# Optimization experiments

Measured on AMD Instinct MI355X. Metric: run time of the kernel, lower is better.

The kernel has to match this reference:

```python
import jax, jax.numpy as jnp
import numpy as np

B, H, KLEN, D = 32, 8, 8192, 64  # batch, heads, kv_len, head_dim


def setup_inputs() -> dict:
    key = jax.random.key(0)
    k1, k2, k3, k4 = jax.random.split(key, 4)
    std = 1.0 / D ** 0.5
    Q = jax.random.normal(k1, (B, H, 1, D), dtype=jnp.float32)
    K = jax.random.normal(k2, (B, H, KLEN, D), dtype=jnp.float32)
    W_c = jax.random.normal(k3, (H, 2 * D, D), dtype=jnp.float32) * std
    W_o = jax.random.normal(k4, (H, D, 1), dtype=jnp.float32) * std
    bias = jnp.zeros((H, 1, D), dtype=jnp.float32)
    return {"Q": Q, "K": K, "W_c": W_c, "W_o": W_o, "bias": bias}


def reference(Q, K, W_c, W_o, bias):
    # concat score (NAIS, He et al. 2018)
    Qe = jnp.broadcast_to(Q, K.shape)                       # [b,h,k,d]
    QK_cat = jnp.concatenate([Qe, K], axis=-1)              # [b,h,k,2d]
    hidden = jax.nn.relu(
        jnp.einsum('bhke,hed->bhkd', QK_cat, W_c) + bias    # bias [h,1,d] broadcasts
    )                                                        # [b,h,k,d]
    scores = jnp.einsum('bhkd,hde->bhk', hidden, W_o)       # sums over d and e(=1)
    return scores
```

## Files before the change

kernel.cpp:

```cpp
#include <hip/hip_runtime.h>
#include <stdint.h>

#define B_    32
#define H_    8
#define KLEN_ 8192
#define D_    64
#define SPLIT 16
#define ROWS_PER_BLOCK (KLEN_ / SPLIT)
#define WAVES 4
#define TILES (ROWS_PER_BLOCK / (WAVES * 16))

#define LDS_ROW 144

typedef __attribute__((ext_vector_type(8))) short short8;
typedef __attribute__((ext_vector_type(4))) float float4v;
typedef __attribute__((ext_vector_type(4))) unsigned int uint4v;
typedef __attribute__((ext_vector_type(2))) unsigned int uint2v;

static __device__ inline unsigned int pack_bf16(float x0, float x1) {
    unsigned int a = __builtin_bit_cast(unsigned int, x0) + 0x8000u;
    unsigned int b = __builtin_bit_cast(unsigned int, x1) + 0x8000u;
    return __builtin_amdgcn_perm(b, a, 0x07060302u);
}

__global__ __launch_bounds__(256) void nais_score_kernel(
    const float* __restrict__ Q,
    const float* __restrict__ K,
    const float* __restrict__ Wc,
    const float* __restrict__ Wo,
    const float* __restrict__ bias,
    float* __restrict__ out)
{
    const int blk   = blockIdx.x;
    const int bh    = blk / SPLIT;
    const int split = blk % SPLIT;
    const int h     = bh % H_;
    const int tid   = threadIdx.x;
    const int lane  = tid & 63;
    const int wave  = tid >> 6;
    const int c     = lane & 15;
    const int q     = lane >> 4;

    __shared__ float s_qb[D_];
    __shared__ float s_wo[D_];
    __shared__ unsigned char s_tile[WAVES][16 * LDS_ROW] __attribute__((aligned(16)));

    if (tid < D_) {
        const float* qv = Q + (size_t)bh * D_;
        const float* wq = Wc + (size_t)h * (2 * D_ * D_);
        float acc = bias[h * D_ + tid];
        #pragma unroll 8
        for (int e = 0; e < D_; ++e)
            acc += qv[e] * wq[e * D_ + tid];
        s_qb[tid] = acc;
        s_wo[tid] = Wo[h * D_ + tid];
    }
    __syncthreads();

    const float* wk = Wc + (size_t)h * (2 * D_ * D_) + D_ * D_;
    short8 bfrag[4][2];
    #pragma unroll
    for (int t = 0; t < 4; ++t) {
        const int d = t * 16 + c;
        #pragma unroll
        for (int half = 0; half < 2; ++half) {
            uint4v f;
            #pragma unroll
            for (int j2 = 0; j2 < 4; ++j2) {
                const int e = half * 32 + q * 8 + 2 * j2;
                f[j2] = pack_bf16(wk[(size_t)e * D_ + d], wk[(size_t)(e + 1) * D_ + d]);
            }
            bfrag[t][half] = __builtin_bit_cast(short8, f);
        }
    }

    float qbl[4], wol[4];
    #pragma unroll
    for (int t = 0; t < 4; ++t) {
        qbl[t] = s_qb[t * 16 + c];
        wol[t] = s_wo[t * 16 + c];
    }

    const float* Kb = K + (size_t)bh * KLEN_ * D_ + (size_t)split * ROWS_PER_BLOCK * D_;
    float*       ob = out + (size_t)bh * KLEN_ + (size_t)split * ROWS_PER_BLOCK;
    unsigned char* myTile = s_tile[wave];

    #define TILE_PTR(t) (Kb + (size_t)(((t) * WAVES + wave) * 16) * D_)

    float4v st[2][4];
    #pragma unroll
    for (int j = 0; j < 4; ++j)
        st[0][j] = *(const float4v*)(TILE_PTR(0) + j * 256 + lane * 4);

    for (int t = 0; t < TILES; ++t) {
        const int cb = t & 1, nb = cb ^ 1;
        if (t + 1 < TILES) {
            #pragma unroll
            for (int j = 0; j < 4; ++j)
                st[nb][j] = *(const float4v*)(TILE_PTR(t + 1) + j * 256 + lane * 4);
        }

        #pragma unroll
        for (int j = 0; j < 4; ++j) {
            const int r = j * 4 + q;
            uint2v w;
            w[0] = pack_bf16(st[cb][j][0], st[cb][j][1]);
            w[1] = pack_bf16(st[cb][j][2], st[cb][j][3]);
            *(uint2v*)(myTile + r * LDS_ROW + c * 8) = w;
        }

        short8 af0 = *(const short8*)(myTile + c * LDS_ROW + q * 16);
        short8 af1 = *(const short8*)(myTile + c * LDS_ROW + 64 + q * 16);

        float4v pr = {0.f, 0.f, 0.f, 0.f};
        #pragma unroll
        for (int tt = 0; tt < 4; ++tt) {
            float4v acc = {0.f, 0.f, 0.f, 0.f};
            acc = __builtin_amdgcn_mfma_f32_16x16x32_bf16(af0, bfrag[tt][0], acc, 0, 0, 0);
            acc = __builtin_amdgcn_mfma_f32_16x16x32_bf16(af1, bfrag[tt][1], acc, 0, 0, 0);
            #pragma unroll
            for (int r = 0; r < 4; ++r) {
                float hv = fmaxf(acc[r] + qbl[tt], 0.f);
                pr[r] += hv * wol[tt];
            }
        }

        const int krow = (t * WAVES + wave) * 16;
        #pragma unroll
        for (int r = 0; r < 4; ++r) {
            float v = pr[r];
            v += __shfl_xor(v, 1);
            v += __shfl_xor(v, 2);
            v += __shfl_xor(v, 4);
            v += __shfl_xor(v, 8);
            if (c == r) ob[krow + q * 4 + r] = v;
        }
    }
    #undef TILE_PTR
}

extern "C" void kernel_launch(void* const* d_in, const int* in_sizes, int n_in,
                              void* d_out, int out_size, void* d_ws, size_t ws_size,
                              hipStream_t stream) {
    const float* Q    = (const float*)d_in[0];
    const float* K    = (const float*)d_in[1];
    const float* Wc   = (const float*)d_in[2];
    const float* Wo   = (const float*)d_in[3];
    const float* bias = (const float*)d_in[4];
    float* out = (float*)d_out;

    dim3 grid(B_ * H_ * SPLIT);
    dim3 block(256);
    nais_score_kernel<<<grid, block, 0, stream>>>(Q, K, Wc, Wo, bias, out);
}
```

Measured before the change: 689.1 us.

## Load K fragments directly into MFMA layout, drop LDS staging and syncthreads

```diff
diff --git a/kernel.cpp b/kernel.cpp
--- a/kernel.cpp
+++ b/kernel.cpp
@@ -9,13 +9,12 @@
 #define ROWS_PER_BLOCK (KLEN_ / SPLIT)
 #define WAVES 4
 #define TILES (ROWS_PER_BLOCK / (WAVES * 16))
+#define TSTRIDE (WAVES * 16 * D_)
 
-#define LDS_ROW 144
-
-typedef __attribute__((ext_vector_type(8))) short short8;
-typedef __attribute__((ext_vector_type(4))) float float4v;
+typedef __attribute__((ext_vector_type(8))) short  short8;
+typedef __attribute__((ext_vector_type(8))) float  float8;
+typedef __attribute__((ext_vector_type(4))) float  float4v;
 typedef __attribute__((ext_vector_type(4))) unsigned int uint4v;
-typedef __attribute__((ext_vector_type(2))) unsigned int uint2v;
 
 static __device__ inline unsigned int pack_bf16(float x0, float x1) {
     unsigned int a = __builtin_bit_cast(unsigned int, x0) + 0x8000u;
@@ -23,7 +22,14 @@
     return __builtin_amdgcn_perm(b, a, 0x07060302u);
 }
 
-__global__ __launch_bounds__(256) void nais_score_kernel(
+static __device__ inline short8 pack8(float8 f) {
+    uint4v p;
+    #pragma unroll
+    for (int j = 0; j < 4; ++j) p[j] = pack_bf16(f[2 * j], f[2 * j + 1]);
+    return __builtin_bit_cast(short8, p);
+}
+
+__global__ __launch_bounds__(256, 4) void nais_score_kernel(
     const float* __restrict__ Q,
     const float* __restrict__ K,
     const float* __restrict__ Wc,
@@ -41,23 +47,38 @@
     const int c     = lane & 15;
     const int q     = lane >> 4;
 
-    __shared__ float s_qb[D_];
-    __shared__ float s_wo[D_];
-    __shared__ unsigned char s_tile[WAVES][16 * LDS_ROW] __attribute__((aligned(16)));
+    const float* Kb    = K + (size_t)bh * (KLEN_ * D_) + (size_t)split * (ROWS_PER_BLOCK * D_);
+    const float* lanep = Kb + (size_t)(wave * 16 + c) * D_ + q * 8;
 
-    if (tid < D_) {
-        const float* qv = Q + (size_t)bh * D_;
-        const float* wq = Wc + (size_t)h * (2 * D_ * D_);
-        float acc = bias[h * D_ + tid];
-        #pragma unroll 8
-        for (int e = 0; e < D_; ++e)
-            acc += qv[e] * wq[e * D_ + tid];
-        s_qb[tid] = acc;
-        s_wo[tid] = Wo[h * D_ + tid];
+    float8 f0[2], f1[2];
+    #pragma unroll
+    for (int p = 0; p < 2; ++p) {
+        f0[p] = *(const float8*)(lanep + p * TSTRIDE);
+        f1[p] = *(const float8*)(lanep + p * TSTRIDE + 32);
     }
-    __syncthreads();
 
-    const float* wk = Wc + (size_t)h * (2 * D_ * D_) + D_ * D_;
+    const float* qv = Q  + (size_t)bh * D_;
+    const float* wq = Wc + (size_t)h * (2 * D_ * D_);
+    const float* wk = wq + D_ * D_;
+
+    float a0 = bias[h * D_ + lane], a1 = 0.f, a2 = 0.f, a3 = 0.f;
+    #pragma unroll
+    for (int e = 0; e < D_; e += 4) {
+        a0 += qv[e]     * wq[(e)     * D_ + lane];
+        a1 += qv[e + 1] * wq[(e + 1) * D_ + lane];
+        a2 += qv[e + 2] * wq[(e + 2) * D_ + lane];
+        a3 += qv[e + 3] * wq[(e + 3) * D_ + lane];
+    }
+    const float qp       = (a0 + a1) + (a2 + a3);
+    const float wol_lane = Wo[h * D_ + lane];
+
+    float qbl[4], wol[4];
+    #pragma unroll
+    for (int tt = 0; tt < 4; ++tt) {
+        qbl[tt] = __shfl(qp,       tt * 16 + c);
+        wol[tt] = __shfl(wol_lane, tt * 16 + c);
+    }
+
     short8 bfrag[4][2];
     #pragma unroll
     for (int t = 0; t < 4; ++t) {
@@ -74,69 +95,43 @@
         }
     }
 
-    float qbl[4], wol[4];
+    float* ob = out + (size_t)bh * KLEN_ + (size_t)split * ROWS_PER_BLOCK
+              + wave * 16 + q * 4 + c;
+
     #pragma unroll
-    for (int t = 0; t < 4; ++t) {
-        qbl[t] = s_qb[t * 16 + c];
-        wol[t] = s_wo[t * 16 + c];
-    }
+    for (int t = 0; t < TILES; ++t) {
+        const int cur = t & 1;
+        short8 af0 = pack8(f0[cur]);
+        short8 af1 = pack8(f1[cur]);
 
-    const float* Kb = K + (size_t)bh * KLEN_ * D_ + (size_t)split * ROWS_PER_BLOCK * D_;
-    float*       ob = out + (size_t)bh * KLEN_ + (size_t)split * ROWS_PER_BLOCK;
-    unsigned char* myTile = s_tile[wave];
-
-    #define TILE_PTR(t) (Kb + (size_t)(((t) * WAVES + wave) * 16) * D_)
-
-    float4v st[2][4];
-    #pragma unroll
-    for (int j = 0; j < 4; ++j)
-        st[0][j] = *(const float4v*)(TILE_PTR(0) + j * 256 + lane * 4);
-
-    for (int t = 0; t < TILES; ++t) {
-        const int cb = t & 1, nb = cb ^ 1;
-        if (t + 1 < TILES) {
-            #pragma unroll
-            for (int j = 0; j < 4; ++j)
-                st[nb][j] = *(const float4v*)(TILE_PTR(t + 1) + j * 256 + lane * 4);
+        if (t + 2 < TILES) {
+            f0[cur] = *(const float8*)(lanep + (t + 2) * TSTRIDE);
+            f1[cur] = *(const float8*)(lanep + (t + 2) * TSTRIDE + 32);
         }
-
-        #pragma unroll
-        for (int j = 0; j < 4; ++j) {
-            const int r = j * 4 + q;
-            uint2v w;
-            w[0] = pack_bf16(st[cb][j][0], st[cb][j][1]);
-            w[1] = pack_bf16(st[cb][j][2], st[cb][j][3]);
-            *(uint2v*)(myTile + r * LDS_ROW + c * 8) = w;
-        }
-
-        short8 af0 = *(const short8*)(myTile + c * LDS_ROW + q * 16);
-        short8 af1 = *(const short8*)(myTile + c * LDS_ROW + 64 + q * 16);
 
         float4v pr = {0.f, 0.f, 0.f, 0.f};
         #pragma unroll
         for (int tt = 0; tt < 4; ++tt) {
-            float4v acc = {0.f, 0.f, 0.f, 0.f};
+            float4v acc = {qbl[tt], qbl[tt], qbl[tt], qbl[tt]};
             acc = __builtin_amdgcn_mfma_f32_16x16x32_bf16(af0, bfrag[tt][0], acc, 0, 0, 0);
             acc = __builtin_amdgcn_mfma_f32_16x16x32_bf16(af1, bfrag[tt][1], acc, 0, 0, 0);
             #pragma unroll
-            for (int r = 0; r < 4; ++r) {
-                float hv = fmaxf(acc[r] + qbl[tt], 0.f);
-                pr[r] += hv * wol[tt];
-            }
+            for (int r = 0; r < 4; ++r)
+                pr[r] += fmaxf(acc[r], 0.f) * wol[tt];
         }
 
-        const int krow = (t * WAVES + wave) * 16;
         #pragma unroll
         for (int r = 0; r < 4; ++r) {
-            float v = pr[r];
-            v += __shfl_xor(v, 1);
-            v += __shfl_xor(v, 2);
-            v += __shfl_xor(v, 4);
-            v += __shfl_xor(v, 8);
-            if (c == r) ob[krow + q * 4 + r] = v;
+            pr[r] += __shfl_xor(pr[r], 1);
+            pr[r] += __shfl_xor(pr[r], 2);
+            pr[r] += __shfl_xor(pr[r], 4);
+            pr[r] += __shfl_xor(pr[r], 8);
         }
+        const float v01 = (c & 1) ? pr[1] : pr[0];
+        const float v23 = (c & 1) ? pr[3] : pr[2];
+        const float v   = (c & 2) ? v23 : v01;
+        if (c < 4) ob[t * (WAVES * 16)] = v;
     }
-    #undef TILE_PTR
 }
 
 extern "C" void kernel_launch(void* const* d_in, const int* in_sizes, int n_in,
```

New measurement: 691.7 us. Within noise of the previous version (+0.4%).
